# Optimization experiments

Measured on AMD Instinct MI355X. Metric: run time of the kernel, lower is better.

The kernel has to match this reference:

```python
import jax, jax.numpy as jnp
import numpy as np

B, E, H, NY, NX = 16, 128, 4, 32, 32


def setup_inputs() -> dict:
    key = jax.random.key(0)
    ks = jax.random.split(key, 7)
    w = lambda k, shape: jax.random.normal(k, shape, jnp.float32) * 0.02
    return {
        "x": jax.random.normal(ks[0], (B, E, NY, NX), jnp.float32),
        "Wk": w(ks[1], (E, E)), "bk": jnp.zeros((E,), jnp.float32),
        "Wq": w(ks[2], (E, E)), "bq": jnp.zeros((E,), jnp.float32),
        "Wv": w(ks[3], (E, E)), "bv": jnp.zeros((E,), jnp.float32),
        "Wu": w(ks[4], (E, E)), "bu": jnp.zeros((E,), jnp.float32),
        "pos_enc": w(ks[5], (H, (2 * NY - 1) * (2 * NX - 1))),
    }


def _conv1x1(x, W, b):
    # 1x1 conv == channel-mixing linear: (B,C,y,x) -> (B,O,y,x)
    return jnp.einsum('bcyx,oc->boyx', x, W) + b[None, :, None, None]


def _rel_indices(ny, nx):
    y = jnp.arange(ny)
    x = jnp.arange(nx)
    y1, x1, y2, x2 = jnp.meshgrid(y, x, y, x, indexing='ij')
    idx = (y1 - y2 + ny - 1) * (2 * nx - 1) + (x1 - x2 + nx - 1)
    return idx.reshape(ny * nx, ny * nx)  # (N, N)


def reference(x, Wk, bk, Wq, bq, Wv, bv, Wu, bu, pos_enc):
    b, e, ny, nx = x.shape
    h = pos_enc.shape[0]
    hc = e // h
    n = ny * nx
    scale = hc ** (-0.5)

    keys = _conv1x1(x, Wk, bk).reshape(b, h, hc, n)
    queries = _conv1x1(x, Wq, bq).reshape(b, h, hc, n)
    values = _conv1x1(x, Wv, bv).reshape(b, h, hc, n)

    # att[b,h,k,q] = sum_c keys[b,h,c,k] * queries[b,h,c,q]
    att = jnp.einsum('bhck,bhcq->bhkq', keys, queries) * scale

    # gathered relative position bias: (H, N, N)
    idx = _rel_indices(ny, nx)
    rel = pos_enc[:, idx]
    att = att + rel[None]

    # softmax over the key axis (dim=-2), as in the original
    att = jax.nn.softmax(att, axis=-2)

    out = jnp.einsum('bhck,bhkq->bhcq', values, att).reshape(b, e, ny, nx)
    return _conv1x1(out, Wu, bu)
```

## Files before the change

kernel.cpp:

```cpp
#include <hip/hip_runtime.h>
#include <hip/hip_bf16.h>

#define BN 16
#define EN 128
#define HN 4
#define HCN 32
#define NN 1024
#define POSN 3969

typedef short short8 __attribute__((ext_vector_type(8)));
typedef float f32x4 __attribute__((ext_vector_type(4)));

#define MFMA16(a, b, c) __builtin_amdgcn_mfma_f32_16x16x32_bf16((a), (b), (c), 0, 0, 0)

union Frag {
  short8 s8;
  uint2 u2[2];
  unsigned int u[4];
  unsigned short us[8];
};

__device__ __forceinline__ unsigned short bfbits(float x) {
  union { __hip_bfloat16 h; unsigned short u; } c;
  c.h = __float2bfloat16(x);
  return c.u;
}

__device__ __forceinline__ unsigned int pk2(float lo, float hi) {
  union { __hip_bfloat162 h2; unsigned int u; } c;
  c.h2 = __float22bfloat162_rn(make_float2(lo, hi));
  return c.u;
}

__global__ __launch_bounds__(256) void prep_kernel(
    const float* __restrict__ pos,
    const float* __restrict__ Wk, const float* __restrict__ Wq,
    const float* __restrict__ Wv, const float* __restrict__ Wu,
    unsigned short* __restrict__ bias, Frag* __restrict__ wtab,
    Frag* __restrict__ whitab, Frag* __restrict__ wlotab)
{
  const int b0 = blockIdx.x, t = threadIdx.x;
  if (b0 < 189) {
    const int gid = b0 * 256 + t;
    const int l = gid & 63;
    const int t2 = gid >> 6;
    const int dxi = t2 % 3;
    const int dy31 = (t2 / 3) % 63;
    const int h = t2 / 189;
    const int rowk0 = (l >> 4) * 4, colq = l & 15;
    const float log2e = 1.4426950408889634f;
    unsigned int bits[4];
#pragma unroll
    for (int j = 0; j < 4; ++j) {
      const int dx = (dxi - 1) * 16 + rowk0 + j - colq + 31;
      bits[j] = (unsigned int)bfbits(pos[h * POSN + dy31 * 63 + dx] * log2e);
    }
    uint2 o;
    o.x = bits[0] | (bits[1] << 16);
    o.y = bits[2] | (bits[3] << 16);
    *(uint2*)(bias + (size_t)gid * 4) = o;
  } else if (b0 < 213) {
    const int fid = (b0 - 189) * 256 + t;
    const int z = fid >> 11, rem = fid & 2047;
    const int ot = rem >> 8, ks = (rem >> 6) & 3, l = rem & 63;
    const float* W = (z == 0) ? Wk : (z == 1) ? Wq : Wv;
    const int o = ot * 16 + (l & 15), lq = l >> 4;
    const float* wp = W + (size_t)o * EN + ks * 32 + lq * 4;
    float4 wa = *(const float4*)wp;
    float4 wb2 = *(const float4*)(wp + 16);
    Frag f;
    f.u[0] = pk2(wa.x, wa.y);   f.u[1] = pk2(wa.z, wa.w);
    f.u[2] = pk2(wb2.x, wb2.y); f.u[3] = pk2(wb2.z, wb2.w);
    wtab[fid] = f;
  } else {
    const int fid = (b0 - 213) * 256 + t;
    const int ot = fid >> 8, ks = (fid >> 6) & 3, l = fid & 63;
    const int o = ot * 16 + (l & 15), lq = l >> 4;
    const float* wp = Wu + (size_t)o * EN + ks * 32 + lq * 4;
    float4 wa = *(const float4*)wp;
    float4 wb2 = *(const float4*)(wp + 16);
    float v[8] = {wa.x, wa.y, wa.z, wa.w, wb2.x, wb2.y, wb2.z, wb2.w};
    unsigned short hb[8]; float lf[8];
#pragma unroll
    for (int e = 0; e < 8; ++e) {
      __hip_bfloat16 hh = __float2bfloat16(v[e]);
      union { __hip_bfloat16 h; unsigned short u; } c; c.h = hh;
      hb[e] = c.u;
      lf[e] = v[e] - __bfloat162float(hh);
    }
    Frag fh, fl;
#pragma unroll
    for (int e = 0; e < 4; ++e)
      fh.u[e] = hb[2 * e] | ((unsigned int)hb[2 * e + 1] << 16);
    fl.u[0] = pk2(lf[0], lf[1]); fl.u[1] = pk2(lf[2], lf[3]);
    fl.u[2] = pk2(lf[4], lf[5]); fl.u[3] = pk2(lf[6], lf[7]);
    whitab[fid] = fh;
    wlotab[fid] = fl;
  }
}

__global__ __launch_bounds__(256) void conv_qkv_mfma(
    const float* __restrict__ x, const Frag* __restrict__ wtab,
    const float* __restrict__ bk, __hip_bfloat16* __restrict__ kb,
    const float* __restrict__ bq, __hip_bfloat16* __restrict__ qb,
    const float* __restrict__ bv, __hip_bfloat16* __restrict__ vb)
{
  const int z = blockIdx.z;
  const float* bias = (z == 0) ? bk : (z == 1) ? bq : bv;
  __hip_bfloat16* out = (z == 0) ? kb : (z == 1) ? qb : vb;

  const int n0 = blockIdx.x * 64;
  const int bb = blockIdx.y;
  const int t = threadIdx.x, w = t >> 6, l = t & 63;
  const int l15 = l & 15, lq = l >> 4;

  __shared__ unsigned short xs[64][132];

  {
    const float* xb = x + (size_t)bb * EN * NN + n0;
    const int n = t & 63, cg = (t >> 6) * 4;
#pragma unroll
    for (int i = 0; i < 8; ++i) {
      const int cb = cg + i * 16;
      float a0 = xb[(size_t)(cb + 0) * NN + n];
      float a1 = xb[(size_t)(cb + 1) * NN + n];
      float a2 = xb[(size_t)(cb + 2) * NN + n];
      float a3 = xb[(size_t)(cb + 3) * NN + n];
      uint2 v; v.x = pk2(a0, a1); v.y = pk2(a2, a3);
      *(uint2*)&xs[n][cb] = v;
    }
  }

  Frag wf[2][4];
#pragma unroll
  for (int r = 0; r < 2; ++r)
#pragma unroll
    for (int ks = 0; ks < 4; ++ks)
      wf[r][ks] = wtab[(((size_t)z * 8 + (w * 2 + r)) * 4 + ks) * 64 + l];
  __syncthreads();

  f32x4 acc[2][4];
#pragma unroll
  for (int r = 0; r < 2; ++r)
#pragma unroll
    for (int nt = 0; nt < 4; ++nt) acc[r][nt] = 0.f;

#pragma unroll
  for (int ks = 0; ks < 4; ++ks) {
#pragma unroll
    for (int nt = 0; nt < 4; ++nt) {
      Frag xf;
      xf.u2[0] = *(const uint2*)&xs[nt * 16 + l15][ks * 32 + lq * 4];
      xf.u2[1] = *(const uint2*)&xs[nt * 16 + l15][ks * 32 + lq * 4 + 16];
      if (z < 2) {
        acc[0][nt] = MFMA16(wf[0][ks].s8, xf.s8, acc[0][nt]);
        acc[1][nt] = MFMA16(wf[1][ks].s8, xf.s8, acc[1][nt]);
      } else {
        acc[0][nt] = MFMA16(xf.s8, wf[0][ks].s8, acc[0][nt]);
        acc[1][nt] = MFMA16(xf.s8, wf[1][ks].s8, acc[1][nt]);
      }
    }
  }

  if (z < 2) {
#pragma unroll
    for (int r = 0; r < 2; ++r) {
      const int ob = (w * 2 + r) * 16 + lq * 4;
      const int hh = ob >> 5;
      const int pofs = hh * 32 + ((ob >> 2) & 3) * 8 + ((ob & 16) ? 4 : 0);
      float4 b4 = *(const float4*)(bias + ob);
#pragma unroll
      for (int nt = 0; nt < 4; ++nt) {
        const int n = n0 + nt * 16 + l15;
        f32x4 a = acc[r][nt];
        uint2 o2;
        o2.x = pk2(a[0] + b4.x, a[1] + b4.y);
        o2.y = pk2(a[2] + b4.z, a[3] + b4.w);
        *(uint2*)(out + (size_t)(bb * NN + n) * 128 + pofs) = o2;
      }
    }
  } else {
#pragma unroll
    for (int r = 0; r < 2; ++r) {
      const int o = (w * 2 + r) * 16 + l15;
      const int c = o & 31, hh = o >> 5;
      const float bsc = bias[o];
#pragma unroll
      for (int nt = 0; nt < 4; ++nt) {
        const int nb = n0 + nt * 16 + lq * 4;
        const int kbk = nb >> 5, k32 = nb & 31;
        const int pofs = ((k32 >> 2) & 3) * 8 + ((k32 & 16) ? 4 : 0);
        f32x4 a = acc[r][nt];
        uint2 o2;
        o2.x = pk2(a[0] + bsc, a[1] + bsc);
        o2.y = pk2(a[2] + bsc, a[3] + bsc);
        *(uint2*)(out + ((size_t)((bb * 4 + hh) * 32 + c) * 32 + kbk) * 32 + pofs) = o2;
      }
    }
  }
}

__global__ __launch_bounds__(256, 4) void attn_mfma_kernel(
    const __hip_bfloat16* __restrict__ kp,
    const __hip_bfloat16* __restrict__ qp,
    const __hip_bfloat16* __restrict__ vp,
    const unsigned short* __restrict__ bias,
    float* __restrict__ Op,
    float* __restrict__ lp)
{
  const int bx = blockIdx.x;
  const int qi = bx & 7, s = bx >> 3;
  const int h = blockIdx.y, b = blockIdx.z;
  const int t = threadIdx.x, w = t >> 6, l = t & 63;
  const int l15 = l & 15, lq = l >> 4;

  __shared__ Frag Kf[2][8][64];
  __shared__ Frag Vf[2][8][64];

  const __hip_bfloat16* kBase = kp + (size_t)b * 131072 + h * 32 + (size_t)l15 * 128 + lq * 8;
  const __hip_bfloat16* vBase = vp + (size_t)((b * 4 + h) * 32 + l15) * 1024 + lq * 8;
  const unsigned short* biasB = bias + (size_t)h * 48384 + l * 4;

#define KADDR(CHG, KT) ((const Frag*)(kBase + (size_t)((CHG) * 128 + (KT) * 16) * 128))
#define VADDR(CHG, SL) ((const Frag*)(vBase + (size_t)((SL) >> 2) * 16384 + ((CHG) * 4 + ((SL) & 3)) * 32))

  const int qt0 = qi * 8 + w * 2;
  Frag qf[2];
  qf[0] = *(const Frag*)(qp + (size_t)(b * 1024 + (qt0 + 0) * 16 + l15) * 128 + h * 32 + lq * 8);
  qf[1] = *(const Frag*)(qp + (size_t)(b * 1024 + (qt0 + 1) * 16 + l15) * 128 + h * 32 + lq * 8);
  const int qy[2] = {(qt0 + 0) >> 1, (qt0 + 1) >> 1};
  const int qx1[2] = {(qt0 + 0) & 1, (qt0 + 1) & 1};

  {
    const int chg = s * 4;
    Kf[0][w][l]     = *KADDR(chg, w);
    Kf[0][w + 4][l] = *KADDR(chg, w + 4);
    Vf[0][w][l]     = *VADDR(chg, w);
    Vf[0][w + 4][l] = *VADDR(chg, w + 4);
  }
  __syncthreads();

  f32x4 O[2][2];
#pragma unroll
  for (int mt = 0; mt < 2; ++mt)
#pragma unroll
    for (int nt = 0; nt < 2; ++nt) O[mt][nt] = 0.f;
  f32x4 Lacc[2]; Lacc[0] = 0.f; Lacc[1] = 0.f;

  Frag ones;
  ones.u[0] = 0x3F803F80u; ones.u[1] = 0x3F803F80u;
  ones.u[2] = 0x3F803F80u; ones.u[3] = 0x3F803F80u;

  const float SCALE2 = 0.17677669529663687f * 1.4426950408889634f;

  for (int c4 = 0; c4 < 4; ++c4) {
    const int buf = c4 & 1;
    const int chg = s * 4 + c4;

    Frag kn[2], vn[2];
    if (c4 < 3) {
      kn[0] = *KADDR(chg + 1, w);
      kn[1] = *KADDR(chg + 1, w + 4);
      vn[0] = *VADDR(chg + 1, w);
      vn[1] = *VADDR(chg + 1, w + 4);
    }

#pragma unroll
    for (int hh2 = 0; hh2 < 2; ++hh2) {
      short8 ka[4], va[4];
#pragma unroll
      for (int kt = 0; kt < 4; ++kt) ka[kt] = Kf[buf][hh2 * 4 + kt][l].s8;
#pragma unroll
      for (int mt = 0; mt < 2; ++mt)
#pragma unroll
        for (int kh = 0; kh < 2; ++kh)
          va[mt * 2 + kh] = Vf[buf][mt * 4 + hh2 * 2 + kh][l].s8;

#pragma unroll
      for (int nt = 0; nt < 2; ++nt) {
        uint2 bw[4];
#pragma unroll
        for (int kt = 0; kt < 4; ++kt) {
          const int ktg = chg * 8 + hh2 * 4 + kt;
          const int off = ((ktg >> 1) - qy[nt] + 31) * 768 + ((ktg & 1) - qx1[nt] + 1) * 256;
          bw[kt] = *(const uint2*)(biasB + off);
        }

        __builtin_amdgcn_s_setprio(1);
        f32x4 S[4];
#pragma unroll
        for (int kt = 0; kt < 4; ++kt) {
          f32x4 z = 0.f;
          S[kt] = MFMA16(ka[kt], qf[nt].s8, z);
        }
        __builtin_amdgcn_s_setprio(0);

        Frag B0, B1;
#pragma unroll
        for (int kt = 0; kt < 4; ++kt) {
          const float b0 = __uint_as_float(bw[kt].x << 16);
          const float b1 = __uint_as_float(bw[kt].x & 0xffff0000u);
          const float b2 = __uint_as_float(bw[kt].y << 16);
          const float b3 = __uint_as_float(bw[kt].y & 0xffff0000u);
          float p0 = exp2f(fmaf(S[kt][0], SCALE2, b0));
          float p1 = exp2f(fmaf(S[kt][1], SCALE2, b1));
          float p2 = exp2f(fmaf(S[kt][2], SCALE2, b2));
          float p3 = exp2f(fmaf(S[kt][3], SCALE2, b3));
          unsigned int lo = pk2(p0, p1), hi = pk2(p2, p3);
          if (kt < 2) { B0.u[kt * 2] = lo; B0.u[kt * 2 + 1] = hi; }
          else        { B1.u[(kt - 2) * 2] = lo; B1.u[(kt - 2) * 2 + 1] = hi; }
        }

        __builtin_amdgcn_s_setprio(1);
        O[0][nt] = MFMA16(va[0], B0.s8, O[0][nt]);
        O[0][nt] = MFMA16(va[1], B1.s8, O[0][nt]);
        O[1][nt] = MFMA16(va[2], B0.s8, O[1][nt]);
        O[1][nt] = MFMA16(va[3], B1.s8, O[1][nt]);
        Lacc[nt] = MFMA16(ones.s8, B0.s8, Lacc[nt]);
        Lacc[nt] = MFMA16(ones.s8, B1.s8, Lacc[nt]);
        __builtin_amdgcn_s_setprio(0);
      }
    }

    if (c4 < 3) {
      Kf[buf ^ 1][w][l]     = kn[0];
      Kf[buf ^ 1][w + 4][l] = kn[1];
      Vf[buf ^ 1][w][l]     = vn[0];
      Vf[buf ^ 1][w + 4][l] = vn[1];
      __syncthreads();
    }
  }
#undef KADDR
#undef VADDR

  if (lq == 0) {
#pragma unroll
    for (int nt = 0; nt < 2; ++nt)
      lp[((size_t)(s * 16 + b) * 4 + h) * 1024 + (qt0 + nt) * 16 + l15] = Lacc[nt][0];
  }

  float* ob = Op + (size_t)s * 2097152 + ((size_t)b * EN + h * HCN) * NN;
#pragma unroll
  for (int mt = 0; mt < 2; ++mt)
#pragma unroll
    for (int nt = 0; nt < 2; ++nt)
#pragma unroll
      for (int j = 0; j < 4; ++j)
        ob[(size_t)(mt * 16 + lq * 4 + j) * NN + (qt0 + nt) * 16 + l15] = O[mt][nt][j];
}

__global__ __launch_bounds__(256) void conv_final_mfma(
    const float* __restrict__ Op,
    const float* __restrict__ lp,
    const Frag* __restrict__ whitab, const Frag* __restrict__ wlotab,
    const float* __restrict__ bu, float* __restrict__ out)
{
  const int n0 = blockIdx.x * 32;
  const int bb = blockIdx.y;
  const int t = threadIdx.x, w = t >> 6, l = t & 63;
  const int l15 = l & 15, lq = l >> 4;

  __shared__ unsigned short ahi[32][132];
  __shared__ unsigned short alo[32][132];

  {
    const float* O0 = Op + (size_t)bb * (EN * NN) + n0;
    const float* O1 = O0 + 2097152;
    const float* l0 = lp + (size_t)bb * 4096 + n0;
    const float* l1 = l0 + 65536;
    const int n = t & 31, cg = (t >> 5) * 4;
#pragma unroll
    for (int i = 0; i < 4; ++i) {
      const int cb = cg + i * 32;
      const float rl = 1.0f / (l0[i * 1024 + n] + l1[i * 1024 + n]);
      float a[4]; unsigned short hb[4]; float lf[4];
#pragma unroll
      for (int j = 0; j < 4; ++j) {
        a[j] = (O0[(size_t)(cb + j) * NN + n] + O1[(size_t)(cb + j) * NN + n]) * rl;
        __hip_bfloat16 hh = __float2bfloat16(a[j]);
        union { __hip_bfloat16 h; unsigned short u; } c; c.h = hh;
        hb[j] = c.u;
        lf[j] = a[j] - __bfloat162float(hh);
      }
      uint2 uh; uh.x = hb[0] | ((unsigned int)hb[1] << 16);
                uh.y = hb[2] | ((unsigned int)hb[3] << 16);
      uint2 ul; ul.x = pk2(lf[0], lf[1]); ul.y = pk2(lf[2], lf[3]);
      *(uint2*)&ahi[n][cb] = uh;
      *(uint2*)&alo[n][cb] = ul;
    }
  }

  Frag whi[2][4], wlo[2][4];
#pragma unroll
  for (int r = 0; r < 2; ++r)
#pragma unroll
    for (int ks = 0; ks < 4; ++ks) {
      const int idx = (((w * 2 + r) * 4) + ks) * 64 + l;
      whi[r][ks] = whitab[idx];
      wlo[r][ks] = wlotab[idx];
    }
  __syncthreads();

  f32x4 acc[2][2];
#pragma unroll
  for (int r = 0; r < 2; ++r)
#pragma unroll
    for (int nt = 0; nt < 2; ++nt) acc[r][nt] = 0.f;

#pragma unroll
  for (int ks = 0; ks < 4; ++ks) {
#pragma unroll
    for (int nt = 0; nt < 2; ++nt) {
      Frag ah, al;
      ah.u2[0] = *(const uint2*)&ahi[nt * 16 + l15][ks * 32 + lq * 4];
      ah.u2[1] = *(const uint2*)&ahi[nt * 16 + l15][ks * 32 + lq * 4 + 16];
      al.u2[0] = *(const uint2*)&alo[nt * 16 + l15][ks * 32 + lq * 4];
      al.u2[1] = *(const uint2*)&alo[nt * 16 + l15][ks * 32 + lq * 4 + 16];
#pragma unroll
      for (int r = 0; r < 2; ++r) {
        acc[r][nt] = MFMA16(ah.s8, whi[r][ks].s8, acc[r][nt]);
        acc[r][nt] = MFMA16(al.s8, whi[r][ks].s8, acc[r][nt]);
        acc[r][nt] = MFMA16(ah.s8, wlo[r][ks].s8, acc[r][nt]);
      }
    }
  }

#pragma unroll
  for (int r = 0; r < 2; ++r) {
    const int o = (w * 2 + r) * 16 + l15;
    const float bo = bu[o];
#pragma unroll
    for (int nt = 0; nt < 2; ++nt) {
      const int nb = n0 + nt * 16 + lq * 4;
      f32x4 a = acc[r][nt];
      float4 res = make_float4(a[0] + bo, a[1] + bo, a[2] + bo, a[3] + bo);
      *(float4*)(out + ((size_t)bb * EN + o) * NN + nb) = res;
    }
  }
}

extern "C" void kernel_launch(void* const* d_in, const int* in_sizes, int n_in,
                              void* d_out, int out_size, void* d_ws, size_t ws_size,
                              hipStream_t stream)
{
  const float* x   = (const float*)d_in[0];
  const float* Wk  = (const float*)d_in[1];
  const float* bk  = (const float*)d_in[2];
  const float* Wq  = (const float*)d_in[3];
  const float* bq  = (const float*)d_in[4];
  const float* Wv  = (const float*)d_in[5];
  const float* bv  = (const float*)d_in[6];
  const float* Wu  = (const float*)d_in[7];
  const float* bu  = (const float*)d_in[8];
  const float* pos = (const float*)d_in[9];

  char* ws = (char*)d_ws;
  __hip_bfloat16* kb = (__hip_bfloat16*)(ws);
  __hip_bfloat16* qb = (__hip_bfloat16*)(ws + (size_t)4194304);
  __hip_bfloat16* vb = (__hip_bfloat16*)(ws + (size_t)8388608);
  unsigned short* bias = (unsigned short*)(ws + (size_t)12582912);
  Frag* wtab   = (Frag*)(ws + (size_t)12969984);
  Frag* whitab = (Frag*)(ws + (size_t)13068288);
  Frag* wlotab = (Frag*)(ws + (size_t)13101056);
  float* lp = (float*)(ws + (size_t)13133824);
  float* Op = (float*)(ws + (size_t)13658112);

  prep_kernel<<<221, 256, 0, stream>>>(pos, Wk, Wq, Wv, Wu, bias, wtab, whitab, wlotab);

  dim3 g1(16, BN, 3);
  conv_qkv_mfma<<<g1, 256, 0, stream>>>(x, wtab, bk, kb, bq, qb, bv, vb);

  dim3 g2(16, HN, BN);
  attn_mfma_kernel<<<g2, 256, 0, stream>>>(kb, qb, vb, bias, Op, lp);

  dim3 g3(32, BN);
  conv_final_mfma<<<g3, 256, 0, stream>>>(Op, lp, whitab, wlotab, bu, (float*)d_out);
}
```

Baseline: 58.11 us.

## Store attention partials as bf16 token-major and fuse QKV projections per block

The attention kernel now writes its split-K partial outputs as packed bf16 in a token-major layout instead of fp32 channel-major. The final conv reads these directly as MFMA fragments, applies the softmax normalisation per head, and drops the hi/lo activation split and LDS staging. The QKV conv now loads the x tile once per block and loops over K, Q and V, which removes the 3x re-read of x. The cost is lower precision on the intermediate output and fewer, larger QKV blocks.

```diff
diff --git a/kernel.cpp b/kernel.cpp
--- a/kernel.cpp
+++ b/kernel.cpp
@@ -105,23 +105,19 @@
     const float* __restrict__ bq, __hip_bfloat16* __restrict__ qb,
     const float* __restrict__ bv, __hip_bfloat16* __restrict__ vb)
 {
-  const int z = blockIdx.z;
-  const float* bias = (z == 0) ? bk : (z == 1) ? bq : bv;
-  __hip_bfloat16* out = (z == 0) ? kb : (z == 1) ? qb : vb;
-
-  const int n0 = blockIdx.x * 64;
+  const int n0 = blockIdx.x * 32;
   const int bb = blockIdx.y;
   const int t = threadIdx.x, w = t >> 6, l = t & 63;
   const int l15 = l & 15, lq = l >> 4;
 
-  __shared__ unsigned short xs[64][132];
+  __shared__ unsigned short xs[32][132];
 
   {
     const float* xb = x + (size_t)bb * EN * NN + n0;
-    const int n = t & 63, cg = (t >> 6) * 4;
-#pragma unroll
-    for (int i = 0; i < 8; ++i) {
-      const int cb = cg + i * 16;
+    const int n = t & 31, cg = (t >> 5) * 4;
+#pragma unroll
+    for (int i = 0; i < 4; ++i) {
+      const int cb = cg + i * 32;
       float a0 = xb[(size_t)(cb + 0) * NN + n];
       float a1 = xb[(size_t)(cb + 1) * NN + n];
       float a2 = xb[(size_t)(cb + 2) * NN + n];
@@ -130,71 +126,77 @@
       *(uint2*)&xs[n][cb] = v;
     }
   }
-
-  Frag wf[2][4];
-#pragma unroll
-  for (int r = 0; r < 2; ++r)
-#pragma unroll
-    for (int ks = 0; ks < 4; ++ks)
-      wf[r][ks] = wtab[(((size_t)z * 8 + (w * 2 + r)) * 4 + ks) * 64 + l];
   __syncthreads();
 
-  f32x4 acc[2][4];
-#pragma unroll
-  for (int r = 0; r < 2; ++r)
-#pragma unroll
-    for (int nt = 0; nt < 4; ++nt) acc[r][nt] = 0.f;
-
-#pragma unroll
-  for (int ks = 0; ks < 4; ++ks) {
-#pragma unroll
-    for (int nt = 0; nt < 4; ++nt) {
-      Frag xf;
-      xf.u2[0] = *(const uint2*)&xs[nt * 16 + l15][ks * 32 + lq * 4];
-      xf.u2[1] = *(const uint2*)&xs[nt * 16 + l15][ks * 32 + lq * 4 + 16];
-      if (z < 2) {
-        acc[0][nt] = MFMA16(wf[0][ks].s8, xf.s8, acc[0][nt]);
-        acc[1][nt] = MFMA16(wf[1][ks].s8, xf.s8, acc[1][nt]);
-      } else {
-        acc[0][nt] = MFMA16(xf.s8, wf[0][ks].s8, acc[0][nt]);
-        acc[1][nt] = MFMA16(xf.s8, wf[1][ks].s8, acc[1][nt]);
+#pragma unroll
+  for (int z = 0; z < 3; ++z) {
+    const float* bias = (z == 0) ? bk : (z == 1) ? bq : bv;
+    __hip_bfloat16* out = (z == 0) ? kb : (z == 1) ? qb : vb;
+
+    Frag wf[2][4];
+#pragma unroll
+    for (int r = 0; r < 2; ++r)
+#pragma unroll
+      for (int ks = 0; ks < 4; ++ks)
+        wf[r][ks] = wtab[(((size_t)z * 8 + (w * 2 + r)) * 4 + ks) * 64 + l];
+
+    f32x4 acc[2][2];
+#pragma unroll
+    for (int r = 0; r < 2; ++r)
+#pragma unroll
+      for (int nt = 0; nt < 2; ++nt) acc[r][nt] = 0.f;
+
+#pragma unroll
+    for (int ks = 0; ks < 4; ++ks) {
+#pragma unroll
+      for (int nt = 0; nt < 2; ++nt) {
+        Frag xf;
+        xf.u2[0] = *(const uint2*)&xs[nt * 16 + l15][ks * 32 + lq * 4];
+        xf.u2[1] = *(const uint2*)&xs[nt * 16 + l15][ks * 32 + lq * 4 + 16];
+        if (z < 2) {
+          acc[0][nt] = MFMA16(wf[0][ks].s8, xf.s8, acc[0][nt]);
+          acc[1][nt] = MFMA16(wf[1][ks].s8, xf.s8, acc[1][nt]);
+        } else {
+          acc[0][nt] = MFMA16(xf.s8, wf[0][ks].s8, acc[0][nt]);
+          acc[1][nt] = MFMA16(xf.s8, wf[1][ks].s8, acc[1][nt]);
+        }
       }
     }
-  }
-
-  if (z < 2) {
-#pragma unroll
-    for (int r = 0; r < 2; ++r) {
-      const int ob = (w * 2 + r) * 16 + lq * 4;
-      const int hh = ob >> 5;
-      const int pofs = hh * 32 + ((ob >> 2) & 3) * 8 + ((ob & 16) ? 4 : 0);
-      float4 b4 = *(const float4*)(bias + ob);
-#pragma unroll
-      for (int nt = 0; nt < 4; ++nt) {
-        const int n = n0 + nt * 16 + l15;
-        f32x4 a = acc[r][nt];
-        uint2 o2;
-        o2.x = pk2(a[0] + b4.x, a[1] + b4.y);
-        o2.y = pk2(a[2] + b4.z, a[3] + b4.w);
-        *(uint2*)(out + (size_t)(bb * NN + n) * 128 + pofs) = o2;
+
+    if (z < 2) {
+#pragma unroll
+      for (int r = 0; r < 2; ++r) {
+        const int ob = (w * 2 + r) * 16 + lq * 4;
+        const int hh = ob >> 5;
+        const int pofs = hh * 32 + ((ob >> 2) & 3) * 8 + ((ob & 16) ? 4 : 0);
+        float4 b4 = *(const float4*)(bias + ob);
+#pragma unroll
+        for (int nt = 0; nt < 2; ++nt) {
+          const int n = n0 + nt * 16 + l15;
+          f32x4 a = acc[r][nt];
+          uint2 o2;
+          o2.x = pk2(a[0] + b4.x, a[1] + b4.y);
+          o2.y = pk2(a[2] + b4.z, a[3] + b4.w);
+          *(uint2*)(out + (size_t)(bb * NN + n) * 128 + pofs) = o2;
+        }
       }
-    }
-  } else {
-#pragma unroll
-    for (int r = 0; r < 2; ++r) {
-      const int o = (w * 2 + r) * 16 + l15;
-      const int c = o & 31, hh = o >> 5;
-      const float bsc = bias[o];
-#pragma unroll
-      for (int nt = 0; nt < 4; ++nt) {
-        const int nb = n0 + nt * 16 + lq * 4;
-        const int kbk = nb >> 5, k32 = nb & 31;
-        const int pofs = ((k32 >> 2) & 3) * 8 + ((k32 & 16) ? 4 : 0);
-        f32x4 a = acc[r][nt];
-        uint2 o2;
-        o2.x = pk2(a[0] + bsc, a[1] + bsc);
-        o2.y = pk2(a[2] + bsc, a[3] + bsc);
-        *(uint2*)(out + ((size_t)((bb * 4 + hh) * 32 + c) * 32 + kbk) * 32 + pofs) = o2;
+    } else {
+#pragma unroll
+      for (int r = 0; r < 2; ++r) {
+        const int o = (w * 2 + r) * 16 + l15;
+        const int c = o & 31, hh = o >> 5;
+        const float bsc = bias[o];
+#pragma unroll
+        for (int nt = 0; nt < 2; ++nt) {
+          const int nb = n0 + nt * 16 + lq * 4;
+          const int kbk = nb >> 5, k32 = nb & 31;
+          const int pofs = ((k32 >> 2) & 3) * 8 + ((k32 & 16) ? 4 : 0);
+          f32x4 a = acc[r][nt];
+          uint2 o2;
+          o2.x = pk2(a[0] + bsc, a[1] + bsc);
+          o2.y = pk2(a[2] + bsc, a[3] + bsc);
+          *(uint2*)(out + ((size_t)((bb * 4 + hh) * 32 + c) * 32 + kbk) * 32 + pofs) = o2;
+        }
       }
     }
   }
@@ -205,7 +207,7 @@
     const __hip_bfloat16* __restrict__ qp,
     const __hip_bfloat16* __restrict__ vp,
     const unsigned short* __restrict__ bias,
-    float* __restrict__ Op,
+    __hip_bfloat16* __restrict__ Opb,
     float* __restrict__ lp)
 {
   const int bx = blockIdx.x;
@@ -339,18 +341,21 @@
       lp[((size_t)(s * 16 + b) * 4 + h) * 1024 + (qt0 + nt) * 16 + l15] = Lacc[nt][0];
   }
 
-  float* ob = Op + (size_t)s * 2097152 + ((size_t)b * EN + h * HCN) * NN;
-#pragma unroll
-  for (int mt = 0; mt < 2; ++mt)
-#pragma unroll
-    for (int nt = 0; nt < 2; ++nt)
-#pragma unroll
-      for (int j = 0; j < 4; ++j)
-        ob[(size_t)(mt * 16 + lq * 4 + j) * NN + (qt0 + nt) * 16 + l15] = O[mt][nt][j];
-}
-
-__global__ __launch_bounds__(256) void conv_final_mfma(
-    const float* __restrict__ Op,
+  __hip_bfloat16* obb = Opb + ((size_t)(s * 16 + b) * 1024) * 128 + h * 32 + lq * 8;
+#pragma unroll
+  for (int nt = 0; nt < 2; ++nt) {
+    const int n = (qt0 + nt) * 16 + l15;
+    Frag f;
+    f.u[0] = pk2(O[0][nt][0], O[0][nt][1]);
+    f.u[1] = pk2(O[0][nt][2], O[0][nt][3]);
+    f.u[2] = pk2(O[1][nt][0], O[1][nt][1]);
+    f.u[3] = pk2(O[1][nt][2], O[1][nt][3]);
+    *(Frag*)(obb + (size_t)n * 128) = f;
+  }
+}
+
+__global__ __launch_bounds__(256, 2) void conv_final_mfma(
+    const __hip_bfloat16* __restrict__ Opb,
     const float* __restrict__ lp,
     const Frag* __restrict__ whitab, const Frag* __restrict__ wlotab,
     const float* __restrict__ bu, float* __restrict__ out)
@@ -360,34 +365,12 @@
   const int t = threadIdx.x, w = t >> 6, l = t & 63;
   const int l15 = l & 15, lq = l >> 4;
 
-  __shared__ unsigned short ahi[32][132];
-  __shared__ unsigned short alo[32][132];
-
-  {
-    const float* O0 = Op + (size_t)bb * (EN * NN) + n0;
-    const float* O1 = O0 + 2097152;
-    const float* l0 = lp + (size_t)bb * 4096 + n0;
-    const float* l1 = l0 + 65536;
-    const int n = t & 31, cg = (t >> 5) * 4;
-#pragma unroll
-    for (int i = 0; i < 4; ++i) {
-      const int cb = cg + i * 32;
-      const float rl = 1.0f / (l0[i * 1024 + n] + l1[i * 1024 + n]);
-      float a[4]; unsigned short hb[4]; float lf[4];
-#pragma unroll
-      for (int j = 0; j < 4; ++j) {
-        a[j] = (O0[(size_t)(cb + j) * NN + n] + O1[(size_t)(cb + j) * NN + n]) * rl;
-        __hip_bfloat16 hh = __float2bfloat16(a[j]);
-        union { __hip_bfloat16 h; unsigned short u; } c; c.h = hh;
-        hb[j] = c.u;
-        lf[j] = a[j] - __bfloat162float(hh);
-      }
-      uint2 uh; uh.x = hb[0] | ((unsigned int)hb[1] << 16);
-                uh.y = hb[2] | ((unsigned int)hb[3] << 16);
-      uint2 ul; ul.x = pk2(lf[0], lf[1]); ul.y = pk2(lf[2], lf[3]);
-      *(uint2*)&ahi[n][cb] = uh;
-      *(uint2*)&alo[n][cb] = ul;
-    }
+  __shared__ float rls[4][32];
+  if (t < 128) {
+    const int h = t >> 5, nl = t & 31;
+    const float l0 = lp[((size_t)(0 * 16 + bb) * 4 + h) * 1024 + n0 + nl];
+    const float l1 = lp[((size_t)(1 * 16 + bb) * 4 + h) * 1024 + n0 + nl];
+    rls[h][nl] = 1.0f / (l0 + l1);
   }
 
   Frag whi[2][4], wlo[2][4];
@@ -408,20 +391,31 @@
     for (int nt = 0; nt < 2; ++nt) acc[r][nt] = 0.f;
 
 #pragma unroll
-  for (int ks = 0; ks < 4; ++ks) {
-#pragma unroll
-    for (int nt = 0; nt < 2; ++nt) {
-      Frag ah, al;
-      ah.u2[0] = *(const uint2*)&ahi[nt * 16 + l15][ks * 32 + lq * 4];
-      ah.u2[1] = *(const uint2*)&ahi[nt * 16 + l15][ks * 32 + lq * 4 + 16];
-      al.u2[0] = *(const uint2*)&alo[nt * 16 + l15][ks * 32 + lq * 4];
-      al.u2[1] = *(const uint2*)&alo[nt * 16 + l15][ks * 32 + lq * 4 + 16];
-#pragma unroll
-      for (int r = 0; r < 2; ++r) {
-        acc[r][nt] = MFMA16(ah.s8, whi[r][ks].s8, acc[r][nt]);
-        acc[r][nt] = MFMA16(al.s8, whi[r][ks].s8, acc[r][nt]);
-        acc[r][nt] = MFMA16(ah.s8, wlo[r][ks].s8, acc[r][nt]);
+  for (int s = 0; s < 2; ++s) {
+#pragma unroll
+    for (int h = 0; h < 4; ++h) {
+      Frag a2[2];
+#pragma unroll
+      for (int nt = 0; nt < 2; ++nt) {
+        const int n = n0 + nt * 16 + l15;
+        Frag af = *(const Frag*)(Opb + ((size_t)((s * 16 + bb) * 1024 + n)) * 128 + h * 32 + lq * 8);
+        const float sc = rls[h][nt * 16 + l15];
+        Frag as;
+#pragma unroll
+        for (int e = 0; e < 4; ++e) {
+          const float f0 = __uint_as_float((unsigned int)af.us[2 * e] << 16) * sc;
+          const float f1 = __uint_as_float((unsigned int)af.us[2 * e + 1] << 16) * sc;
+          as.u[e] = pk2(f0, f1);
+        }
+        a2[nt] = as;
       }
+#pragma unroll
+      for (int r = 0; r < 2; ++r)
+#pragma unroll
+        for (int nt = 0; nt < 2; ++nt) {
+          acc[r][nt] = MFMA16(a2[nt].s8, whi[r][h].s8, acc[r][nt]);
+          acc[r][nt] = MFMA16(a2[nt].s8, wlo[r][h].s8, acc[r][nt]);
+        }
     }
   }
 
@@ -463,16 +457,16 @@
   Frag* whitab = (Frag*)(ws + (size_t)13068288);
   Frag* wlotab = (Frag*)(ws + (size_t)13101056);
   float* lp = (float*)(ws + (size_t)13133824);
-  float* Op = (float*)(ws + (size_t)13658112);
+  __hip_bfloat16* Opb = (__hip_bfloat16*)(ws + (size_t)13658112);
 
   prep_kernel<<<221, 256, 0, stream>>>(pos, Wk, Wq, Wv, Wu, bias, wtab, whitab, wlotab);
 
-  dim3 g1(16, BN, 3);
+  dim3 g1(32, BN);
   conv_qkv_mfma<<<g1, 256, 0, stream>>>(x, wtab, bk, kb, bq, qb, bv, vb);
 
   dim3 g2(16, HN, BN);
-  attn_mfma_kernel<<<g2, 256, 0, stream>>>(kb, qb, vb, bias, Op, lp);
+  attn_mfma_kernel<<<g2, 256, 0, stream>>>(kb, qb, vb, bias, Opb, lp);
 
   dim3 g3(32, BN);
-  conv_final_mfma<<<g3, 256, 0, stream>>>(Op, lp, whitab, wlotab, bu, (float*)d_out);
-}
+  conv_final_mfma<<<g3, 256, 0, stream>>>(Opb, lp, whitab, wlotab, bu, (float*)d_out);
+}
```

New measurement: 59.30 us. 2.0% more time.
